# Performance work log

Measured on AMD Instinct MI355X. Metric: run time of the kernel, lower is better.

The kernel has to match this reference:

```python
import jax, jax.numpy as jnp
import numpy as np

L = 2        # n_layers
F = 128      # in_features == out_features (GRUCell + highway constraint)
O = 128
N = 1024     # nodes
B = 8        # batch
D = 3        # edge directions (weight.size(0))


def setup_inputs() -> dict:
    key = jax.random.key(0)
    ks = jax.random.split(key, 10)
    s = 1.0 / np.sqrt(F)
    u = lambda k, shp: jax.random.uniform(k, shp, jnp.float32, minval=-s, maxval=s)
    return {
        "inputs": jax.random.normal(ks[0], (N, B, F), jnp.float32),
        "adj": jax.random.uniform(ks[1], (D, B, N, N), jnp.float32),
        "W": u(ks[2], (L, D, F, O)),            # GCN weight per layer/direction
        "Bc": u(ks[3], (L, D, O)),              # GCN bias
        "Wh": u(ks[4], (L, F, O)),              # highway weight
        "Bh": u(ks[5], (L, O)),                 # highway bias
        "Wih": u(ks[6], (L, 3 * O, O)),         # GRUCell input weights
        "Whh": u(ks[7], (L, 3 * O, O)),         # GRUCell hidden weights
        "bih": u(ks[8], (L, 3 * O)),
        "bhh": u(ks[9], (L, 3 * O)),
    }


def _gru(x, h, wih, whh, bih, bhh):
    # torch.nn.GRUCell semantics; x,h: [..., O]
    gi = x @ wih.T + bih
    gh = h @ whh.T + bhh
    i_r, i_z, i_n = jnp.split(gi, 3, axis=-1)
    h_r, h_z, h_n = jnp.split(gh, 3, axis=-1)
    r = jax.nn.sigmoid(i_r + h_r)
    z = jax.nn.sigmoid(i_z + h_z)
    n = jnp.tanh(i_n + r * h_n)
    return (1.0 - z) * n + z * h


def reference(inputs, adj, W, Bc, Wh, Bh, Wih, Whh, bih, bhh):
    x = inputs  # [N, B, F]; dropout layers are identity at eval
    for l in range(L):
        # support per direction: [D, B, N, O]
        support = jnp.einsum('nbf,dfo->dbno', x, W[l]) + Bc[l][:, None, None, :]
        # adjacency-weighted aggregation: adj[d,b] @ support[d,b]
        agg = jnp.einsum('dbmn,dbno->dbmo', adj, support)
        # GRU update with hidden = current features, per direction, summed over d
        h = jnp.broadcast_to(jnp.transpose(x, (1, 0, 2))[None], agg.shape)
        hnew = _gru(agg, h, Wih[l], Whh[l], bih[l], bhh[l])
        out = jnp.transpose(jnp.sum(hnew, axis=0), (1, 0, 2))  # [N, B, O]
        out = jax.nn.relu(out)  # activation='relu'
        # highway gate (highway='relu')
        t = jax.nn.relu(jnp.einsum('nbf,fo->nbo', x, Wh[l]) + Bh[l])
        x = out * t + x * (1.0 - t)
    return x
```

## Files before the change

### kernel.cpp

```cpp
#include <hip/hip_runtime.h>
#include <math.h>

#define N_NODES 1024
#define BATCH   8
#define FEAT    128
#define NDIR    3
#define NB      (N_NODES*BATCH)
#define G3      384

typedef __bf16 bf16_t;
using bf16x8 = __attribute__((ext_vector_type(8))) __bf16;
using bf16x4 = __attribute__((ext_vector_type(4))) __bf16;
using f32x4  = __attribute__((ext_vector_type(4))) float;

#define GLOAD_LDS16(g, l) \
    __builtin_amdgcn_global_load_lds((const __attribute__((address_space(1))) void*)(g), \
                                     (__attribute__((address_space(3))) void*)(l), 16, 0, 0)

template<int R>
__device__ __forceinline__ void stage_op(const bf16_t* __restrict__ src, int stride,
                                         int k0, bf16_t* lds, int w, int lane)
{
    #pragma unroll
    for (int q = 0; q < R/32; ++q) {
        int rbase = w*(R/4) + q*8;
        int row = rbase + (lane >> 3);
        int seg = lane & 7;
        GLOAD_LDS16(src + (size_t)row*stride + k0 + seg*8,
                    (char*)lds + (size_t)rbase*128);
    }
}

template<int MI, int NJ>
__device__ __forceinline__ void mfma_tile(const bf16_t* As, const bf16_t* Bs,
                                          f32x4 (&acc)[MI][NJ], int wr, int wc, int lane)
{
    #pragma unroll
    for (int ks = 0; ks < 64; ks += 32) {
        bf16x8 af[MI], bf[NJ];
        #pragma unroll
        for (int i = 0; i < MI; ++i)
            af[i] = *reinterpret_cast<const bf16x8*>(
                &As[(wr*MI*16 + i*16 + (lane & 15))*64 + ks + ((lane >> 4) * 8)]);
        #pragma unroll
        for (int j = 0; j < NJ; ++j)
            bf[j] = *reinterpret_cast<const bf16x8*>(
                &Bs[(wc*NJ*16 + j*16 + (lane & 15))*64 + ks + ((lane >> 4) * 8)]);
        #pragma unroll
        for (int i = 0; i < MI; ++i) {
            #pragma unroll
            for (int j = 0; j < NJ; ++j)
                acc[i][j] = __builtin_amdgcn_mfma_f32_16x16x32_bf16(af[i], bf[j], acc[i][j], 0, 0, 0);
        }
    }
}

__global__ __launch_bounds__(256) void k_cvt_adj(
    const float* __restrict__ src, bf16_t* __restrict__ dst, int n4)
{
    int i = blockIdx.x * 256 + threadIdx.x;
    int stride = gridDim.x * 256;
    for (; i < n4; i += stride) {
        float4 v = reinterpret_cast<const float4*>(src)[i];
        bf16x4 o;
        o[0] = (bf16_t)(v.x - 0.5f); o[1] = (bf16_t)(v.y - 0.5f);
        o[2] = (bf16_t)(v.z - 0.5f); o[3] = (bf16_t)(v.w - 0.5f);
        *reinterpret_cast<bf16x4*>(&dst[(size_t)i * 4]) = o;
    }
}

__global__ __launch_bounds__(128) void k_wprep(
    const float* __restrict__ W, const float* __restrict__ Wh,
    const float* __restrict__ Whh, const float* __restrict__ Wih,
    bf16_t* __restrict__ wsup,
    bf16_t* __restrict__ wihc)
{
    int m = blockIdx.x, l = blockIdx.y, k = threadIdx.x;
    float w;
    bf16_t* dst;
    bool patB = false;
    if (m < 384) {
        int d = m >> 7, o = m & 127;
        w = W[((size_t)(l*3 + d)*128 + k)*128 + o];
        dst = wsup + ((size_t)l*896 + m)*384;
    } else if (m < 512) {
        int o = m - 384;
        w = Wh[((size_t)l*128 + k)*128 + o];
        dst = wsup + ((size_t)l*896 + m)*384;
    } else if (m < 896) {
        int c = m - 512;
        w = Whh[((size_t)l*384 + c)*128 + k];
        dst = wsup + ((size_t)l*896 + m)*384;
    } else {
        int c = m - 896;
        w = Wih[((size_t)l*384 + c)*128 + k];
        dst = wihc + ((size_t)l*384 + c)*384;
        patB = true;
    }
    bf16_t hi = (bf16_t)w;
    bf16_t lo = (bf16_t)(w - (float)hi);
    if (patB) { dst[k] = hi; dst[128 + k] = hi; dst[256 + k] = lo; }
    else      { dst[k] = hi; dst[128 + k] = lo; dst[256 + k] = hi; }
}

__global__ __launch_bounds__(256) void k_xcat(
    const float* __restrict__ X, bf16_t* __restrict__ xcat)
{
    int idx = blockIdx.x * 256 + threadIdx.x;
    int k = idx & 127, r = idx >> 7;
    int n = r >> 3, b = r & 7;
    float v = X[idx];
    bf16_t hi = (bf16_t)v;
    bf16_t lo = (bf16_t)(v - (float)hi);
    bf16_t* dst = xcat + ((size_t)(b*1024 + n))*384 + k;
    dst[0] = hi; dst[128] = hi; dst[256] = lo;
}

__global__ __launch_bounds__(256, 2) void k_sup2(
    const bf16_t* __restrict__ Wcat,
    const bf16_t* __restrict__ xcat,
    const float* __restrict__ Bcl,
    const float* __restrict__ Bhl,
    const float* __restrict__ bhhl,
    bf16_t* __restrict__ supt,
    float* __restrict__ tbuf,
    bf16_t* __restrict__ ghb)
{
    __shared__ bf16_t As[128*64];
    __shared__ bf16_t Bs[128*64];
    const int t = threadIdx.x, lane = t & 63, w = t >> 6;
    const int wr = w >> 1, wc = w & 1;
    const int n0 = blockIdx.x * 128;
    const int m0 = blockIdx.y * 128;
    const int b  = blockIdx.z;
    const bf16_t* Arow = Wcat + (size_t)m0 * 384;
    const bf16_t* Brow = xcat + ((size_t)b * 1024 + n0) * 384;

    f32x4 acc[4][4] = {};
    for (int k0 = 0; k0 < 384; k0 += 64) {
        stage_op<128>(Arow, 384, k0, As, w, lane);
        stage_op<128>(Brow, 384, k0, Bs, w, lane);
        __syncthreads();
        mfma_tile<4,4>(As, Bs, acc, wr, wc, lane);
        __syncthreads();
    }
    #pragma unroll
    for (int i = 0; i < 4; ++i) {
        int mb = m0 + wr*64 + i*16 + ((lane >> 4) * 4);
        #pragma unroll
        for (int j = 0; j < 4; ++j) {
            int n = n0 + wc*64 + j*16 + (lane & 15);
            if (mb < 384) {
                #pragma unroll
                for (int rg = 0; rg < 4; ++rg) {
                    int m = mb + rg;
                    int d = m >> 7, o = m & 127;
                    supt[((size_t)((d*8 + b)*128 + o))*1024 + n] =
                        (bf16_t)(acc[i][j][rg] + Bcl[d*128 + o]);
                }
            } else if (mb < 512) {
                #pragma unroll
                for (int rg = 0; rg < 4; ++rg) {
                    int o = mb + rg - 384;
                    tbuf[((size_t)(b*128 + o))*1024 + n] =
                        fmaxf(acc[i][j][rg] + Bhl[o], 0.0f);
                }
            } else {
                int c = mb - 512;
                bf16x4 pk;
                #pragma unroll
                for (int rg = 0; rg < 4; ++rg)
                    pk[rg] = (bf16_t)(acc[i][j][rg] + bhhl[c + rg]);
                *reinterpret_cast<bf16x4*>(&ghb[((size_t)(b*1024 + n))*384 + c]) = pk;
            }
        }
    }
}

__global__ __launch_bounds__(256) void k_colsum(
    const bf16_t* __restrict__ supt, float* __restrict__ colsum)
{
    int row = blockIdx.x * 4 + (threadIdx.x >> 6);
    int lane = threadIdx.x & 63;
    const bf16_t* p = supt + (size_t)row * 1024 + lane * 16;
    bf16x8 v0 = *reinterpret_cast<const bf16x8*>(p);
    bf16x8 v1 = *reinterpret_cast<const bf16x8*>(p + 8);
    float s = 0.0f;
    #pragma unroll
    for (int i = 0; i < 8; ++i) s += (float)v0[i] + (float)v1[i];
    #pragma unroll
    for (int off = 32; off > 0; off >>= 1) s += __shfl_down(s, off, 64);
    if (lane == 0) colsum[row] = s;
}

__global__ __launch_bounds__(256, 2) void k_agg(
    const bf16_t* __restrict__ adjb,
    const bf16_t* __restrict__ supt,
    const float* __restrict__ colsum,
    bf16_t* __restrict__ aggcat)
{
    __shared__ bf16_t As[64*64];
    __shared__ bf16_t Bs[128*64];
    const int t = threadIdx.x, lane = t & 63, w = t >> 6;
    const int wr = w >> 1, wc = w & 1;
    const int m0 = blockIdx.x * 64;
    const int z  = blockIdx.y;
    const bf16_t* Arow = adjb + (size_t)z * 1024 * 1024 + (size_t)m0 * 1024;
    const bf16_t* Brow = supt + (size_t)z * 128 * 1024;

    f32x4 acc[2][4] = {};
    for (int k0 = 0; k0 < 1024; k0 += 64) {
        stage_op<64>(Arow, 1024, k0, As, w, lane);
        stage_op<128>(Brow, 1024, k0, Bs, w, lane);
        __syncthreads();
        mfma_tile<2,4>(As, Bs, acc, wr, wc, lane);
        __syncthreads();
    }
    #pragma unroll
    for (int i = 0; i < 2; ++i) {
        #pragma unroll
        for (int rg = 0; rg < 4; ++rg) {
            size_t m = (size_t)z*1024 + m0 + wr*32 + i*16 + ((lane >> 4) * 4) + rg;
            bf16_t* row = aggcat + m*384;
            #pragma unroll
            for (int j = 0; j < 4; ++j) {
                int o = wc*64 + j*16 + (lane & 15);
                float v = acc[i][j][rg] + 0.5f * colsum[z*128 + o];
                bf16_t hi = (bf16_t)v;
                bf16_t lo = (bf16_t)(v - (float)hi);
                row[o] = hi; row[128 + o] = lo; row[256 + o] = hi;
            }
        }
    }
}

__global__ __launch_bounds__(256, 2) void k_gi(
    const bf16_t* __restrict__ A,
    const bf16_t* __restrict__ B,
    const float*  __restrict__ bias,
    bf16_t* __restrict__ girz,
    float* __restrict__ gin)
{
    __shared__ bf16_t As[128*64];
    __shared__ bf16_t Bs[128*64];
    const int t = threadIdx.x, lane = t & 63, w = t >> 6;
    const int wr = w >> 1, wc = w & 1;
    const int m0 = blockIdx.x * 128;
    const int c0 = blockIdx.y * 128;
    const bf16_t* Arow = A + (size_t)m0 * 384;
    const bf16_t* Brow = B + (size_t)c0 * 384;

    f32x4 acc[4][4] = {};
    for (int k0 = 0; k0 < 384; k0 += 64) {
        stage_op<128>(Arow, 384, k0, As, w, lane);
        stage_op<128>(Brow, 384, k0, Bs, w, lane);
        __syncthreads();
        mfma_tile<4,4>(As, Bs, acc, wr, wc, lane);
        __syncthreads();
    }
    #pragma unroll
    for (int j = 0; j < 4; ++j) {
        int c = c0 + wc*64 + j*16 + (lane & 15);
        float bv = bias[c];
        #pragma unroll
        for (int i = 0; i < 4; ++i) {
            #pragma unroll
            for (int rg = 0; rg < 4; ++rg) {
                int m = m0 + wr*64 + i*16 + ((lane >> 4) * 4) + rg;
                float v = acc[i][j][rg] + bv;
                if (c < 256) girz[(size_t)m*256 + c] = (bf16_t)v;
                else         gin[(size_t)m*128 + (c - 256)] = v;
            }
        }
    }
}

__global__ __launch_bounds__(256) void k_gates(
    const bf16_t* __restrict__ girz, const float* __restrict__ gin,
    const bf16_t* __restrict__ ghb,
    bf16_t* xcat,
    const float* __restrict__ tbuf,
    float* __restrict__ Xout, int write_xcat)
{
    __shared__ float ts[128*17];
    const int b = blockIdx.y, n0 = blockIdx.x * 16;
    const int tid = threadIdx.x;
    {
        int o = tid >> 1, nh = (tid & 1) * 8;
        const float* src = tbuf + ((size_t)(b*128 + o))*1024 + n0 + nh;
        float4 v0 = *reinterpret_cast<const float4*>(src);
        float4 v1 = *reinterpret_cast<const float4*>(src + 4);
        float* dst = &ts[o*17 + nh];
        dst[0]=v0.x; dst[1]=v0.y; dst[2]=v0.z; dst[3]=v0.w;
        dst[4]=v1.x; dst[5]=v1.y; dst[6]=v1.z; dst[7]=v1.w;
    }
    __syncthreads();
    #pragma unroll
    for (int p = 0; p < 8; ++p) {
        int e = p*256 + tid;
        int nn = e >> 7, o = e & 127;
        int n = n0 + nn;
        size_t rb = (size_t)(b*1024 + n);
        bf16_t* xr = xcat + rb*384;
        float h = (float)xr[o] + (float)xr[256 + o];
        const bf16_t* ghr = ghb + rb*G3;
        float g_r = (float)ghr[o], g_z = (float)ghr[128+o], g_n = (float)ghr[256+o];
        float acc = 0.0f;
        #pragma unroll
        for (int d = 0; d < 3; ++d) {
            size_t rr = (size_t)((d*8 + b)*1024 + n);
            float i_r = (float)girz[rr*256 + o];
            float i_z = (float)girz[rr*256 + 128 + o];
            float i_n = gin[rr*128 + o];
            float rg = 1.0f / (1.0f + expf(-(i_r + g_r)));
            float zg = 1.0f / (1.0f + expf(-(i_z + g_z)));
            float ng = tanhf(i_n + rg * g_n);
            acc += (1.0f - zg) * ng + zg * h;
        }
        float outv = fmaxf(acc, 0.0f);
        float tg = ts[o*17 + nn];
        float res = outv * tg + h * (1.0f - tg);
        if (Xout) Xout[(size_t)(n*8 + b)*128 + o] = res;
        if (write_xcat) {
            bf16_t hi = (bf16_t)res;
            bf16_t lo = (bf16_t)(res - (float)hi);
            xr[o] = hi; xr[128 + o] = hi; xr[256 + o] = lo;
        }
    }
}

extern "C" void kernel_launch(void* const* d_in, const int* in_sizes, int n_in,
                              void* d_out, int out_size, void* d_ws, size_t ws_size,
                              hipStream_t stream) {
    const float* inputs = (const float*)d_in[0];
    const float* adj    = (const float*)d_in[1];
    const float* W      = (const float*)d_in[2];
    const float* Bc     = (const float*)d_in[3];
    const float* Wh     = (const float*)d_in[4];
    const float* Bh     = (const float*)d_in[5];
    const float* Wih    = (const float*)d_in[6];
    const float* Whh    = (const float*)d_in[7];
    const float* bih    = (const float*)d_in[8];
    const float* bhh    = (const float*)d_in[9];

    char* ws = (char*)d_ws;
    float*  tbuf   = (float*)ws;   ws += (size_t)8*128*1024*4;
    bf16_t* xcat   = (bf16_t*)ws;  ws += (size_t)8*1024*384*2;
    bf16_t* ghb    = (bf16_t*)ws;  ws += (size_t)NB*G3*2;
    bf16_t* supt   = (bf16_t*)ws;  ws += (size_t)24*128*1024*2;
    bf16_t* aggcat = (bf16_t*)ws;  ws += (size_t)3*NB*384*2;
    bf16_t* girz   = (bf16_t*)ws;  ws += (size_t)3*NB*256*2;
    float*  gin    = (float*)ws;   ws += (size_t)3*NB*128*4;
    float*  colsum = (float*)ws;   ws += (size_t)24*128*4;
    bf16_t* wsup   = (bf16_t*)ws;  ws += (size_t)2*896*384*2;
    bf16_t* wihc   = (bf16_t*)ws;  ws += (size_t)2*384*384*2;
    bf16_t* adjb   = (bf16_t*)ws;

    k_cvt_adj<<<dim3(4096), dim3(256), 0, stream>>>(adj, adjb, 3*8*1024*1024/4);
    k_wprep<<<dim3(1280, 2), dim3(128), 0, stream>>>(W, Wh, Whh, Wih, wsup, wihc);
    k_xcat<<<dim3(4096), dim3(256), 0, stream>>>(inputs, xcat);

    for (int l = 0; l < 2; ++l) {
        k_sup2<<<dim3(8, 7, 8), dim3(256), 0, stream>>>(
            wsup + (size_t)l*896*384, xcat, Bc + l*3*128, Bh + l*128, bhh + l*G3,
            supt, tbuf, ghb);
        k_colsum<<<dim3(768), dim3(256), 0, stream>>>(supt, colsum);
        k_agg<<<dim3(16, 24), dim3(256), 0, stream>>>(adjb, supt, colsum, aggcat);
        k_gi<<<dim3(192, 3), dim3(256), 0, stream>>>(
            aggcat, wihc + (size_t)l*384*384, bih + l*G3, girz, gin);
        k_gates<<<dim3(64, 8), dim3(256), 0, stream>>>(
            girz, gin, ghb, xcat, tbuf,
            (l == 1) ? (float*)d_out : (float*)nullptr, (l == 0) ? 1 : 0);
    }
}
```

Before: 332.2 us.

## Double-buffer GEMM tiles with XOR-swizzled LDS and fuse adj conversion into agg

All three GEMM kernels now double-buffer their LDS tiles, issuing the loads for the next K-tile before computing the current one, with one barrier per iteration instead of two. LDS tiles are stored with an XOR swizzle so the MFMA fragment reads avoid bank conflicts. The separate fp32-to-bf16 adjacency conversion pass is removed. The layer-0 aggregation kernel instead reads fp32 adj directly, converts it in registers, and writes the bf16 copy back for layer 1. This removes one full pass over the 100 MB adjacency, but layer-0 A staging becomes synchronous register loads and LDS use doubles, which may lower occupancy.

```diff
diff --git a/kernel.cpp b/kernel.cpp
--- a/kernel.cpp
+++ b/kernel.cpp
@@ -18,54 +18,67 @@
                                      (__attribute__((address_space(3))) void*)(l), 16, 0, 0)
 
 template<int R>
-__device__ __forceinline__ void stage_op(const bf16_t* __restrict__ src, int stride,
-                                         int k0, bf16_t* lds, int w, int lane)
+__device__ __forceinline__ void stage_swz(const bf16_t* __restrict__ src, int stride,
+                                          int k0, bf16_t* lds, int w, int lane)
 {
     #pragma unroll
     for (int q = 0; q < R/32; ++q) {
         int rbase = w*(R/4) + q*8;
         int row = rbase + (lane >> 3);
-        int seg = lane & 7;
+        int seg = (lane & 7) ^ (row & 7);
         GLOAD_LDS16(src + (size_t)row*stride + k0 + seg*8,
                     (char*)lds + (size_t)rbase*128);
     }
 }
 
+__device__ __forceinline__ void stageA_f32(const float* __restrict__ src, int k0,
+                                           bf16_t* lds, bf16_t* __restrict__ gout,
+                                           int w, int lane)
+{
+    #pragma unroll
+    for (int q = 0; q < 2; ++q) {
+        int rbase = w*16 + q*8;
+        int row = rbase + (lane >> 3);
+        int s   = lane & 7;
+        int seg = s ^ (row & 7);
+        const float* g = src + (size_t)row*1024 + k0 + seg*8;
+        float4 v0 = *reinterpret_cast<const float4*>(g);
+        float4 v1 = *reinterpret_cast<const float4*>(g + 4);
+        bf16x8 pk;
+        pk[0]=(bf16_t)(v0.x-0.5f); pk[1]=(bf16_t)(v0.y-0.5f);
+        pk[2]=(bf16_t)(v0.z-0.5f); pk[3]=(bf16_t)(v0.w-0.5f);
+        pk[4]=(bf16_t)(v1.x-0.5f); pk[5]=(bf16_t)(v1.y-0.5f);
+        pk[6]=(bf16_t)(v1.z-0.5f); pk[7]=(bf16_t)(v1.w-0.5f);
+        *reinterpret_cast<bf16x8*>(&lds[row*64 + s*8]) = pk;
+        *reinterpret_cast<bf16x8*>(gout + (size_t)row*1024 + k0 + seg*8) = pk;
+    }
+}
+
 template<int MI, int NJ>
-__device__ __forceinline__ void mfma_tile(const bf16_t* As, const bf16_t* Bs,
-                                          f32x4 (&acc)[MI][NJ], int wr, int wc, int lane)
+__device__ __forceinline__ void mfma_swz(const bf16_t* As, const bf16_t* Bs,
+                                         f32x4 (&acc)[MI][NJ], int wr, int wc, int lane)
 {
     #pragma unroll
     for (int ks = 0; ks < 64; ks += 32) {
-        bf16x8 af[MI], bf[NJ];
-        #pragma unroll
-        for (int i = 0; i < MI; ++i)
-            af[i] = *reinterpret_cast<const bf16x8*>(
-                &As[(wr*MI*16 + i*16 + (lane & 15))*64 + ks + ((lane >> 4) * 8)]);
-        #pragma unroll
-        for (int j = 0; j < NJ; ++j)
-            bf[j] = *reinterpret_cast<const bf16x8*>(
-                &Bs[(wc*NJ*16 + j*16 + (lane & 15))*64 + ks + ((lane >> 4) * 8)]);
+        int bslot = ks/8 + (lane >> 4);
+        int sx = bslot ^ (lane & 7);
+        bf16x8 af[MI], bfv[NJ];
+        #pragma unroll
+        for (int i = 0; i < MI; ++i) {
+            int row = wr*MI*16 + i*16 + (lane & 15);
+            af[i] = *reinterpret_cast<const bf16x8*>(&As[row*64 + sx*8]);
+        }
+        #pragma unroll
+        for (int j = 0; j < NJ; ++j) {
+            int row = wc*NJ*16 + j*16 + (lane & 15);
+            bfv[j] = *reinterpret_cast<const bf16x8*>(&Bs[row*64 + sx*8]);
+        }
         #pragma unroll
         for (int i = 0; i < MI; ++i) {
             #pragma unroll
             for (int j = 0; j < NJ; ++j)
-                acc[i][j] = __builtin_amdgcn_mfma_f32_16x16x32_bf16(af[i], bf[j], acc[i][j], 0, 0, 0);
-        }
-    }
-}
-
-__global__ __launch_bounds__(256) void k_cvt_adj(
-    const float* __restrict__ src, bf16_t* __restrict__ dst, int n4)
-{
-    int i = blockIdx.x * 256 + threadIdx.x;
-    int stride = gridDim.x * 256;
-    for (; i < n4; i += stride) {
-        float4 v = reinterpret_cast<const float4*>(src)[i];
-        bf16x4 o;
-        o[0] = (bf16_t)(v.x - 0.5f); o[1] = (bf16_t)(v.y - 0.5f);
-        o[2] = (bf16_t)(v.z - 0.5f); o[3] = (bf16_t)(v.w - 0.5f);
-        *reinterpret_cast<bf16x4*>(&dst[(size_t)i * 4]) = o;
+                acc[i][j] = __builtin_amdgcn_mfma_f32_16x16x32_bf16(af[i], bfv[j], acc[i][j], 0, 0, 0);
+        }
     }
 }
 
@@ -126,8 +139,8 @@
     float* __restrict__ tbuf,
     bf16_t* __restrict__ ghb)
 {
-    __shared__ bf16_t As[128*64];
-    __shared__ bf16_t Bs[128*64];
+    __shared__ bf16_t As[2][128*64];
+    __shared__ bf16_t Bs[2][128*64];
     const int t = threadIdx.x, lane = t & 63, w = t >> 6;
     const int wr = w >> 1, wc = w & 1;
     const int n0 = blockIdx.x * 128;
@@ -137,11 +150,16 @@
     const bf16_t* Brow = xcat + ((size_t)b * 1024 + n0) * 384;
 
     f32x4 acc[4][4] = {};
-    for (int k0 = 0; k0 < 384; k0 += 64) {
-        stage_op<128>(Arow, 384, k0, As, w, lane);
-        stage_op<128>(Brow, 384, k0, Bs, w, lane);
-        __syncthreads();
-        mfma_tile<4,4>(As, Bs, acc, wr, wc, lane);
+    stage_swz<128>(Arow, 384, 0, As[0], w, lane);
+    stage_swz<128>(Brow, 384, 0, Bs[0], w, lane);
+    __syncthreads();
+    #pragma unroll
+    for (int kt = 0; kt < 6; ++kt) {
+        if (kt + 1 < 6) {
+            stage_swz<128>(Arow, 384, (kt+1)*64, As[(kt+1)&1], w, lane);
+            stage_swz<128>(Brow, 384, (kt+1)*64, Bs[(kt+1)&1], w, lane);
+        }
+        mfma_swz<4,4>(As[kt&1], Bs[kt&1], acc, wr, wc, lane);
         __syncthreads();
     }
     #pragma unroll
@@ -193,27 +211,37 @@
     if (lane == 0) colsum[row] = s;
 }
 
+template<int AMODE>
 __global__ __launch_bounds__(256, 2) void k_agg(
-    const bf16_t* __restrict__ adjb,
+    const float* __restrict__ adjf,
+    bf16_t* __restrict__ adjb,
     const bf16_t* __restrict__ supt,
     const float* __restrict__ colsum,
     bf16_t* __restrict__ aggcat)
 {
-    __shared__ bf16_t As[64*64];
-    __shared__ bf16_t Bs[128*64];
+    __shared__ bf16_t As[2][64*64];
+    __shared__ bf16_t Bs[2][128*64];
     const int t = threadIdx.x, lane = t & 63, w = t >> 6;
     const int wr = w >> 1, wc = w & 1;
     const int m0 = blockIdx.x * 64;
     const int z  = blockIdx.y;
-    const bf16_t* Arow = adjb + (size_t)z * 1024 * 1024 + (size_t)m0 * 1024;
+    const float*  Af = adjf + (size_t)z * 1024 * 1024 + (size_t)m0 * 1024;
+    bf16_t*       Ab = adjb + (size_t)z * 1024 * 1024 + (size_t)m0 * 1024;
     const bf16_t* Brow = supt + (size_t)z * 128 * 1024;
 
     f32x4 acc[2][4] = {};
-    for (int k0 = 0; k0 < 1024; k0 += 64) {
-        stage_op<64>(Arow, 1024, k0, As, w, lane);
-        stage_op<128>(Brow, 1024, k0, Bs, w, lane);
-        __syncthreads();
-        mfma_tile<2,4>(As, Bs, acc, wr, wc, lane);
+    if (AMODE) stageA_f32(Af, 0, As[0], Ab, w, lane);
+    else       stage_swz<64>(Ab, 1024, 0, As[0], w, lane);
+    stage_swz<128>(Brow, 1024, 0, Bs[0], w, lane);
+    __syncthreads();
+    #pragma unroll
+    for (int kt = 0; kt < 16; ++kt) {
+        if (kt + 1 < 16) {
+            if (AMODE) stageA_f32(Af, (kt+1)*64, As[(kt+1)&1], Ab, w, lane);
+            else       stage_swz<64>(Ab, 1024, (kt+1)*64, As[(kt+1)&1], w, lane);
+            stage_swz<128>(Brow, 1024, (kt+1)*64, Bs[(kt+1)&1], w, lane);
+        }
+        mfma_swz<2,4>(As[kt&1], Bs[kt&1], acc, wr, wc, lane);
         __syncthreads();
     }
     #pragma unroll
@@ -241,8 +269,8 @@
     bf16_t* __restrict__ girz,
     float* __restrict__ gin)
 {
-    __shared__ bf16_t As[128*64];
-    __shared__ bf16_t Bs[128*64];
+    __shared__ bf16_t As[2][128*64];
+    __shared__ bf16_t Bs[2][128*64];
     const int t = threadIdx.x, lane = t & 63, w = t >> 6;
     const int wr = w >> 1, wc = w & 1;
     const int m0 = blockIdx.x * 128;
@@ -251,11 +279,16 @@
     const bf16_t* Brow = B + (size_t)c0 * 384;
 
     f32x4 acc[4][4] = {};
-    for (int k0 = 0; k0 < 384; k0 += 64) {
-        stage_op<128>(Arow, 384, k0, As, w, lane);
-        stage_op<128>(Brow, 384, k0, Bs, w, lane);
-        __syncthreads();
-        mfma_tile<4,4>(As, Bs, acc, wr, wc, lane);
+    stage_swz<128>(Arow, 384, 0, As[0], w, lane);
+    stage_swz<128>(Brow, 384, 0, Bs[0], w, lane);
+    __syncthreads();
+    #pragma unroll
+    for (int kt = 0; kt < 6; ++kt) {
+        if (kt + 1 < 6) {
+            stage_swz<128>(Arow, 384, (kt+1)*64, As[(kt+1)&1], w, lane);
+            stage_swz<128>(Brow, 384, (kt+1)*64, Bs[(kt+1)&1], w, lane);
+        }
+        mfma_swz<4,4>(As[kt&1], Bs[kt&1], acc, wr, wc, lane);
         __syncthreads();
     }
     #pragma unroll
@@ -356,7 +389,6 @@
     bf16_t* wihc   = (bf16_t*)ws;  ws += (size_t)2*384*384*2;
     bf16_t* adjb   = (bf16_t*)ws;
 
-    k_cvt_adj<<<dim3(4096), dim3(256), 0, stream>>>(adj, adjb, 3*8*1024*1024/4);
     k_wprep<<<dim3(1280, 2), dim3(128), 0, stream>>>(W, Wh, Whh, Wih, wsup, wihc);
     k_xcat<<<dim3(4096), dim3(256), 0, stream>>>(inputs, xcat);
 
@@ -365,7 +397,10 @@
             wsup + (size_t)l*896*384, xcat, Bc + l*3*128, Bh + l*128, bhh + l*G3,
             supt, tbuf, ghb);
         k_colsum<<<dim3(768), dim3(256), 0, stream>>>(supt, colsum);
-        k_agg<<<dim3(16, 24), dim3(256), 0, stream>>>(adjb, supt, colsum, aggcat);
+        if (l == 0)
+            k_agg<1><<<dim3(16, 24), dim3(256), 0, stream>>>(adj, adjb, supt, colsum, aggcat);
+        else
+            k_agg<0><<<dim3(16, 24), dim3(256), 0, stream>>>(adj, adjb, supt, colsum, aggcat);
         k_gi<<<dim3(192, 3), dim3(256), 0, stream>>>(
             aggcat, wihc + (size_t)l*384*384, bih + l*G3, girz, gin);
         k_gates<<<dim3(64, 8), dim3(256), 0, stream>>>(
```

Measured after the change: 331.9 us. Within noise of the previous version (-0.1%).
